# Kernel tuning notes

Measured on AMD Instinct MI355X. Metric: run time of the kernel, lower is better.

The kernel has to match this reference:

```python
import jax, jax.numpy as jnp
import numpy as np

T = 4            # timesteps (init arg T)
K = 8            # num_thresholds
B = 64           # batch per timestep (x.shape[0] == T*B)


def setup_inputs() -> dict:
    key = jax.random.key(0)
    kx, = jax.random.split(key, 1)
    x = jax.random.normal(kx, (T * B, 128, 32, 32), dtype=jnp.float32)
    thresh = jnp.asarray(1.0, dtype=jnp.float32)  # scalar learnable threshold
    return {"x": x, "thresh": thresh}


def reference(x, thresh):
    # thre_shaped: thresh / 2**k, shaped [K, 1,1,1,1] to broadcast over mem[None] = [1,B,C,H,W]
    thre = (thresh / (2.0 ** jnp.arange(K, dtype=x.dtype))).reshape((K,) + (1,) * x.ndim)
    thr75 = thre * 0.75

    xt = x.reshape((T, x.shape[0] // T) + x.shape[1:])  # expand: [T, B, C, H, W]

    def step(mem, xc):
        mem = mem + xc
        # which thresholds the membrane exceeds (thresholds are decreasing in k)
        pos = (mem[None] >= thr75).astype(x.dtype)           # [K, B, C, H, W]
        pos_true = pos.at[1:].add(-pos[:-1])                 # first (largest) crossed threshold only
        spike = jnp.sum(thre * pos_true, axis=0)             # [B, C, H, W]
        return mem - spike, spike

    mem0 = jnp.zeros_like(xt[0])
    _, spikes = jax.lax.scan(step, mem0, xt)                 # spikes: [T, B, C, H, W]
    return spikes.reshape(x.shape)                            # merge: [T*B, C, H, W]
```

## Files before the change

### kernel.cpp

```cpp
#include <hip/hip_runtime.h>


constexpr int T_STEPS = 4;
constexpr int BLOCK = 256;
constexpr int NXCD = 8;

typedef float v4f __attribute__((ext_vector_type(4)));

__device__ __forceinline__ float spike_of(float mem, int b75_0, int b75_7, int bth0) {
    int u = __float_as_int(mem);
    int d = (int)((unsigned)b75_0 - (unsigned)u);
    int k = (int)((unsigned)d + 0x7fffffu) >> 23;
    k = k > 0 ? k : 0;
    int sb = bth0 - (k << 23);
    return (u >= b75_7) ? __int_as_float(sb) : 0.0f;
}

__global__ __launch_bounds__(BLOCK) void snn_mth_kernel(
    const float* __restrict__ x,
    const float* __restrict__ p_thresh,
    float* __restrict__ out,
    int s4)
{
    const float thresh = *p_thresh;
    const int bth0  = __float_as_int(thresh);
    const int b75_0 = __float_as_int(0.75f * thresh);
    const int b75_7 = b75_0 - 7 * 0x800000;

    const v4f* __restrict__ xv = reinterpret_cast<const v4f*>(x);
    v4f* __restrict__ ov = reinterpret_cast<v4f*>(out);

    const int seg_cols   = s4 / (NXCD * BLOCK) * BLOCK;
    const int seg_blocks = seg_cols / BLOCK;
    const int main_blocks = seg_blocks * NXCD;

    const int b = blockIdx.x;
    size_t j;
    if (b < main_blocks) {
        const int xcd  = b % NXCD;
        const int slot = b / NXCD;
        j = (size_t)xcd * seg_cols + (size_t)slot * BLOCK + threadIdx.x;
    } else {
        j = (size_t)NXCD * seg_cols + (size_t)(b - main_blocks) * BLOCK + threadIdx.x;
        if (j >= (size_t)s4) return;
    }

    const size_t n = (size_t)s4;

    v4f xc[T_STEPS];
#pragma unroll
    for (int t = 0; t < T_STEPS; ++t)
        xc[t] = xv[(size_t)t * n + j];

    v4f sp[T_STEPS];
#pragma unroll
    for (int e = 0; e < 4; ++e) {
        float mem = xc[0][e];
        float s0 = spike_of(mem, b75_0, b75_7, bth0);
        sp[0][e] = s0;
        mem = mem - s0 + xc[1][e];
        float s1 = spike_of(mem, b75_0, b75_7, bth0);
        sp[1][e] = s1;
        mem = mem - s1 + xc[2][e];
        float s2 = spike_of(mem, b75_0, b75_7, bth0);
        sp[2][e] = s2;
        mem = mem - s2 + xc[3][e];
        sp[3][e] = spike_of(mem, b75_0, b75_7, bth0);
    }

#pragma unroll
    for (int t = 0; t < T_STEPS; ++t)
        __builtin_nontemporal_store(sp[t], &ov[(size_t)t * n + j]);
}

extern "C" void kernel_launch(void* const* d_in, const int* in_sizes, int n_in,
                              void* d_out, int out_size, void* d_ws, size_t ws_size,
                              hipStream_t stream) {
    const float* x = (const float*)d_in[0];
    const float* p_thresh = (const float*)d_in[1];
    float* out = (float*)d_out;

    const int total = in_sizes[0];
    const int S = total / T_STEPS;
    const int s4 = S >> 2;

    const int grid = (s4 + BLOCK - 1) / BLOCK;
    snn_mth_kernel<<<grid, BLOCK, 0, stream>>>(x, p_thresh, out, s4);
}
```

Measured before the change: 233.9 us.

## Process four chunks per block with double-buffered register loads

Each block now handles four BLOCK-sized chunks instead of one, using two register buffers so the loads for the next chunk are issued before the current chunk is computed and stored. The XCD-aware block-to-chunk mapping is generalised to spread any grid size evenly across the eight XCDs. The aim is to keep more memory requests in flight per wave and to cut block launch overhead. In exchange the kernel uses more registers, which may lower occupancy, and runs a quarter as many blocks.

```diff
diff --git a/kernel.cpp b/kernel.cpp
--- a/kernel.cpp
+++ b/kernel.cpp
@@ -2,8 +2,10 @@
 
 
 constexpr int T_STEPS = 4;
-constexpr int BLOCK = 256;
-constexpr int NXCD = 8;
+constexpr int BLOCK   = 256;
+constexpr int UNROLL  = 4;
+constexpr int CHUNK   = BLOCK * UNROLL;
+constexpr int NXCD    = 8;
 
 typedef float v4f __attribute__((ext_vector_type(4)));
 
@@ -30,47 +32,59 @@
     const v4f* __restrict__ xv = reinterpret_cast<const v4f*>(x);
     v4f* __restrict__ ov = reinterpret_cast<v4f*>(out);
 
-    const int seg_cols   = s4 / (NXCD * BLOCK) * BLOCK;
-    const int seg_blocks = seg_cols / BLOCK;
-    const int main_blocks = seg_blocks * NXCD;
+    const int nwg  = (int)gridDim.x;
+    const int b    = (int)blockIdx.x;
+    const int q    = nwg / NXCD, r = nwg % NXCD;
+    const int xcd  = b % NXCD;
+    const int slot = b / NXCD;
+    const int c    = (xcd < r ? xcd * (q + 1) : r * (q + 1) + (xcd - r) * q) + slot;
 
-    const int b = blockIdx.x;
-    size_t j;
-    if (b < main_blocks) {
-        const int xcd  = b % NXCD;
-        const int slot = b / NXCD;
-        j = (size_t)xcd * seg_cols + (size_t)slot * BLOCK + threadIdx.x;
-    } else {
-        j = (size_t)NXCD * seg_cols + (size_t)(b - main_blocks) * BLOCK + threadIdx.x;
-        if (j >= (size_t)s4) return;
-    }
+    const size_t n    = (size_t)s4;
+    const size_t base = (size_t)c * CHUNK + threadIdx.x;
 
-    const size_t n = (size_t)s4;
+    v4f bufA[T_STEPS], bufB[T_STEPS];
 
-    v4f xc[T_STEPS];
+    auto LOAD = [&](v4f (&buf)[T_STEPS], int i) {
+        const size_t j = base + (size_t)i * BLOCK;
+        if (j < n) {
 #pragma unroll
-    for (int t = 0; t < T_STEPS; ++t)
-        xc[t] = xv[(size_t)t * n + j];
+            for (int t = 0; t < T_STEPS; ++t)
+                buf[t] = xv[(size_t)t * n + j];
+        }
+    };
 
-    v4f sp[T_STEPS];
+    auto PROC = [&](v4f (&buf)[T_STEPS], int i) {
+        const size_t j = base + (size_t)i * BLOCK;
+        if (j < n) {
+            v4f sp[T_STEPS];
 #pragma unroll
-    for (int e = 0; e < 4; ++e) {
-        float mem = xc[0][e];
-        float s0 = spike_of(mem, b75_0, b75_7, bth0);
-        sp[0][e] = s0;
-        mem = mem - s0 + xc[1][e];
-        float s1 = spike_of(mem, b75_0, b75_7, bth0);
-        sp[1][e] = s1;
-        mem = mem - s1 + xc[2][e];
-        float s2 = spike_of(mem, b75_0, b75_7, bth0);
-        sp[2][e] = s2;
-        mem = mem - s2 + xc[3][e];
-        sp[3][e] = spike_of(mem, b75_0, b75_7, bth0);
-    }
+            for (int e = 0; e < 4; ++e) {
+                float mem = buf[0][e];
+                float s0 = spike_of(mem, b75_0, b75_7, bth0);
+                sp[0][e] = s0;
+                mem = mem - s0 + buf[1][e];
+                float s1 = spike_of(mem, b75_0, b75_7, bth0);
+                sp[1][e] = s1;
+                mem = mem - s1 + buf[2][e];
+                float s2 = spike_of(mem, b75_0, b75_7, bth0);
+                sp[2][e] = s2;
+                mem = mem - s2 + buf[3][e];
+                sp[3][e] = spike_of(mem, b75_0, b75_7, bth0);
+            }
+#pragma unroll
+            for (int t = 0; t < T_STEPS; ++t)
+                __builtin_nontemporal_store(sp[t], &ov[(size_t)t * n + j]);
+        }
+    };
 
-#pragma unroll
-    for (int t = 0; t < T_STEPS; ++t)
-        __builtin_nontemporal_store(sp[t], &ov[(size_t)t * n + j]);
+    LOAD(bufA, 0);
+    LOAD(bufB, 1);
+    PROC(bufA, 0);
+    LOAD(bufA, 2);
+    PROC(bufB, 1);
+    LOAD(bufB, 3);
+    PROC(bufA, 2);
+    PROC(bufB, 3);
 }
 
 extern "C" void kernel_launch(void* const* d_in, const int* in_sizes, int n_in,
@@ -84,6 +98,6 @@
     const int S = total / T_STEPS;
     const int s4 = S >> 2;
 
-    const int grid = (s4 + BLOCK - 1) / BLOCK;
+    const int grid = (s4 + CHUNK - 1) / CHUNK;
     snn_mth_kernel<<<grid, BLOCK, 0, stream>>>(x, p_thresh, out, s4);
 }
```

After: 278.6 us. +19.1%, slower.
